# Kernel tuning notes

Hardware: AMD Instinct MI355X
Metric: run time of the kernel (lower is better)

## Reference

```python
import jax, jax.numpy as jnp
import numpy as np

M, K, N = 8192, 4096, 4096


def setup_inputs() -> dict:
    key = jax.random.key(0)
    k1, k2, k3, k4 = jax.random.split(key, 4)
    x = jax.random.normal(k1, (M, K), dtype=jnp.float32)
    # int8 weight buffer (qweight), per-output-channel dequant scales, bf16-style bias
    weight_q = jax.random.randint(k2, (N, K), -128, 128, dtype=jnp.int32).astype(jnp.int8)
    qscales = jax.random.uniform(k3, (N,), dtype=jnp.float32) * 0.01 + 0.005
    bias = jax.random.normal(k4, (N,), dtype=jnp.float32) * 0.01
    return {"x": x, "weight_q": weight_q, "qscales": qscales, "bias": bias}


def reference(x, weight_q, qscales, bias):
    # dynamic per-tensor activation quantization: clampv = max(x)
    clampv = jnp.max(x)
    x8 = jnp.clip(jnp.round(x * (127.0 / clampv)), -128, 127).astype(jnp.int8)
    acc = jax.lax.dot_general(
        x8, weight_q,
        dimension_numbers=(((1,), (1,)), ((), ())),
        preferred_element_type=jnp.int32,
    )
    # fused dequant: (acc*alpha + bias/qscales)*qscales == acc*alpha*qscales + bias
    out = acc.astype(jnp.float32) * (clampv / 127.0) * qscales[None, :] + bias[None, :]
    return out
```

## Files before the change

kernel.cpp:

```cpp
#include <hip/hip_runtime.h>
#include <math.h>

#define MDIM 8192
#define KDIM 4096
#define NDIM 4096

typedef int v4i __attribute__((ext_vector_type(4)));

__device__ __forceinline__ void gload_lds16(const void* g, void* l) {
  __builtin_amdgcn_global_load_lds(
      (const __attribute__((address_space(1))) void*)g,
      (__attribute__((address_space(3))) void*)l,
      16, 0, 0);
}

__global__ void __launch_bounds__(256) kmax(const float* __restrict__ x,
                                            unsigned int* __restrict__ key_out) {
  const int n4 = MDIM * KDIM / 4;
  int tid = blockIdx.x * blockDim.x + threadIdx.x;
  int stride = gridDim.x * blockDim.x;
  float m = -3.4e38f;
  const float4* x4 = (const float4*)x;
  for (int i = tid; i < n4; i += stride) {
    float4 v = x4[i];
    m = fmaxf(m, fmaxf(fmaxf(v.x, v.y), fmaxf(v.z, v.w)));
  }
  #pragma unroll
  for (int off = 32; off > 0; off >>= 1)
    m = fmaxf(m, __shfl_down(m, off, 64));
  __shared__ float sm[4];
  int lane = threadIdx.x & 63, wv = threadIdx.x >> 6;
  if (lane == 0) sm[wv] = m;
  __syncthreads();
  if (threadIdx.x == 0) {
    m = fmaxf(fmaxf(sm[0], sm[1]), fmaxf(sm[2], sm[3]));
    unsigned b = __float_as_uint(m);
    unsigned key = (b & 0x80000000u) ? ~b : (b | 0x80000000u);
    atomicMax(key_out, key);
  }
}

__device__ __forceinline__ float key_to_float(unsigned key) {
  unsigned b = (key & 0x80000000u) ? (key & 0x7FFFFFFFu) : ~key;
  return __uint_as_float(b);
}

__global__ void __launch_bounds__(256) kpackw(const int* __restrict__ w,
                                              signed char* __restrict__ w8) {
  __shared__ int smode;
  int ok = 1;
  #pragma unroll
  for (int i = 0; i < 16; ++i) {
    int v = w[threadIdx.x * 16 + i];
    ok &= (v >= -128) & (v <= 127);
  }
  if (threadIdx.x == 0) smode = 1;
  __syncthreads();
  if (!ok) atomicAnd(&smode, 0);
  __syncthreads();
  const int mode = smode;

  const int n16 = NDIM * KDIM / 16;
  int tid = blockIdx.x * blockDim.x + threadIdx.x;
  int stride = gridDim.x * blockDim.x;
  int4* dst = (int4*)w8;
  if (mode) {
    const int4* src = (const int4*)w;
    for (int i = tid; i < n16; i += stride) {
      int4 r;
      #pragma unroll
      for (int q = 0; q < 4; ++q) {
        int4 a = src[(size_t)i * 4 + q];
        int packed = (a.x & 255) | ((a.y & 255) << 8) |
                     ((a.z & 255) << 16) | ((a.w & 255) << 24);
        ((int*)&r)[q] = packed;
      }
      dst[i] = r;
    }
  } else {
    const int4* src = (const int4*)w;
    for (int i = tid; i < n16; i += stride) dst[i] = src[i];
  }
}

__device__ __forceinline__ int pack4(float4 v, float s) {
  int q0 = (int)fminf(fmaxf(rintf(v.x * s), -128.f), 127.f);
  int q1 = (int)fminf(fmaxf(rintf(v.y * s), -128.f), 127.f);
  int q2 = (int)fminf(fmaxf(rintf(v.z * s), -128.f), 127.f);
  int q3 = (int)fminf(fmaxf(rintf(v.w * s), -128.f), 127.f);
  return (q0 & 255) | ((q1 & 255) << 8) | ((q2 & 255) << 16) | ((q3 & 255) << 24);
}

__global__ void __launch_bounds__(256) kquant(const float* __restrict__ x,
                                              signed char* __restrict__ x8,
                                              const unsigned* __restrict__ keyp) {
  float s = 127.0f / key_to_float(*keyp);
  const int n16 = MDIM * KDIM / 16;
  int tid = blockIdx.x * blockDim.x + threadIdx.x;
  int stride = gridDim.x * blockDim.x;
  const float4* x4 = (const float4*)x;
  int4* out16 = (int4*)x8;
  for (int i = tid; i < n16; i += stride) {
    const float4* src = x4 + (size_t)i * 4;
    int4 r;
    r.x = pack4(src[0], s);
    r.y = pack4(src[1], s);
    r.z = pack4(src[2], s);
    r.w = pack4(src[3], s);
    out16[i] = r;
  }
}

constexpr int BM = 256, BN = 256, BK = 128;
constexpr int NT = KDIM / BK;

__device__ __forceinline__ v4i mfma_i8(v4i a, v4i b, v4i c) {
  return __builtin_amdgcn_mfma_i32_16x16x64_i8(a, b, c, 0, 0, 0);
}

#define PHASE_END()                                         \
  do {                                                      \
    asm volatile("s_waitcnt vmcnt(10)" ::: "memory");       \
    __builtin_amdgcn_s_barrier();                           \
    __builtin_amdgcn_sched_barrier(0);                      \
  } while (0)

__global__ void __launch_bounds__(512, 2) kgemm(
    const signed char* __restrict__ A8,
    const signed char* __restrict__ W8,
    const float* __restrict__ qs,
    const float* __restrict__ bias,
    const unsigned* __restrict__ keyp,
    float* __restrict__ out) {
  __shared__ alignas(1024) signed char lds[2][2][2][128 * 128];

  const int nbn = NDIM / BN;
  const int nwg = (MDIM / BM) * nbn;
  int bid = blockIdx.x;
  int wg = (bid & 7) * (nwg / 8) + (bid >> 3);
  const int brow = (wg / nbn) * BM;
  const int bcol = (wg % nbn) * BN;

  const int tid = threadIdx.x;
  const int lane = tid & 63;
  const int wv = tid >> 6;
  const int wr = wv >> 2, wc = wv & 3;
  const int lhi = lane >> 4, llo = lane & 15;

  const signed char* Abase = A8 + (size_t)brow * KDIM;
  const signed char* Bbase = W8 + (size_t)bcol * KDIM;

  auto stageA = [&](int t, int h) {
    signed char* dst = &lds[t & 1][0][h][0];
    const size_t k0 = (size_t)(t & (NT - 1)) * BK;
    #pragma unroll
    for (int l = 0; l < 2; ++l) {
      int p = l * 512 + tid;
      int r = p >> 3, s = p & 7;
      int R = ((r >> 6) << 7) + h * 64 + (r & 63);
      int g = s ^ (r & 7);
      gload_lds16(Abase + (size_t)R * KDIM + k0 + g * 16, dst + p * 16);
    }
  };
  auto stageB = [&](int t, int h) {
    signed char* dst = &lds[t & 1][1][h][0];
    const size_t k0 = (size_t)(t & (NT - 1)) * BK;
    #pragma unroll
    for (int l = 0; l < 2; ++l) {
      int p = l * 512 + tid;
      int r = p >> 3, s = p & 7;
      int R = ((r >> 5) << 6) + h * 32 + (r & 31);
      int g = s ^ (r & 7);
      gload_lds16(Bbase + (size_t)R * KDIM + k0 + g * 16, dst + p * 16);
    }
  };
  auto readA = [&](int par, int mi, int ks) -> v4i {
    int h = mi >> 2;
    int r = wr * 64 + (mi & 3) * 16 + llo;
    int s = (ks * 4 + lhi) ^ (llo & 7);
    return *(const v4i*)&lds[par][0][h][r * 128 + s * 16];
  };
  auto readB = [&](int par, int ni, int ks) -> v4i {
    int h = ni >> 1;
    int r = wc * 32 + (ni & 1) * 16 + llo;
    int s = (ks * 4 + lhi) ^ (llo & 7);
    return *(const v4i*)&lds[par][1][h][r * 128 + s * 16];
  };

  v4i acc[8][4];
  v4i zero = {0, 0, 0, 0};
  #pragma unroll
  for (int i = 0; i < 8; ++i)
    #pragma unroll
    for (int j = 0; j < 4; ++j) acc[i][j] = zero;

  stageA(0, 0); stageB(0, 0); stageB(0, 1); stageA(0, 1);
  stageA(1, 0); stageB(1, 0); stageB(1, 1);
  asm volatile("s_waitcnt vmcnt(6)" ::: "memory");
  __builtin_amdgcn_s_barrier();
  __builtin_amdgcn_sched_barrier(0);

  #pragma unroll 2
  for (int t = 0; t < NT; ++t) {
    const int par = t & 1;
    v4i afr03[4][2], afr47[4][2], bfr01[2][2], bfr23[2][2];

    #pragma unroll
    for (int mi = 0; mi < 4; ++mi) {
      afr03[mi][0] = readA(par, mi, 0);
      afr03[mi][1] = readA(par, mi, 1);
    }
    #pragma unroll
    for (int ni = 0; ni < 2; ++ni) {
      bfr01[ni][0] = readB(par, ni, 0);
      bfr01[ni][1] = readB(par, ni, 1);
    }
    stageA(t + 1, 1);
    __builtin_amdgcn_s_barrier();
    __builtin_amdgcn_sched_barrier(0);
    __builtin_amdgcn_s_setprio(1);
    #pragma unroll
    for (int mi = 0; mi < 4; ++mi)
      #pragma unroll
      for (int ni = 0; ni < 2; ++ni) {
        acc[mi][ni] = mfma_i8(afr03[mi][0], bfr01[ni][0], acc[mi][ni]);
        acc[mi][ni] = mfma_i8(afr03[mi][1], bfr01[ni][1], acc[mi][ni]);
      }
    __builtin_amdgcn_s_setprio(0);
    PHASE_END();

    #pragma unroll
    for (int ni = 0; ni < 2; ++ni) {
      bfr23[ni][0] = readB(par, 2 + ni, 0);
      bfr23[ni][1] = readB(par, 2 + ni, 1);
    }
    stageA(t + 2, 0);
    __builtin_amdgcn_s_barrier();
    __builtin_amdgcn_sched_barrier(0);
    __builtin_amdgcn_s_setprio(1);
    #pragma unroll
    for (int mi = 0; mi < 4; ++mi)
      #pragma unroll
      for (int ni = 0; ni < 2; ++ni) {
        acc[mi][2 + ni] = mfma_i8(afr03[mi][0], bfr23[ni][0], acc[mi][2 + ni]);
        acc[mi][2 + ni] = mfma_i8(afr03[mi][1], bfr23[ni][1], acc[mi][2 + ni]);
      }
    __builtin_amdgcn_s_setprio(0);
    PHASE_END();

    #pragma unroll
    for (int mi = 0; mi < 4; ++mi) {
      afr47[mi][0] = readA(par, 4 + mi, 0);
      afr47[mi][1] = readA(par, 4 + mi, 1);
    }
    stageB(t + 2, 0);
    __builtin_amdgcn_s_barrier();
    __builtin_amdgcn_sched_barrier(0);
    __builtin_amdgcn_s_setprio(1);
    #pragma unroll
    for (int mi = 0; mi < 4; ++mi)
      #pragma unroll
      for (int ni = 0; ni < 2; ++ni) {
        acc[4 + mi][ni] = mfma_i8(afr47[mi][0], bfr01[ni][0], acc[4 + mi][ni]);
        acc[4 + mi][ni] = mfma_i8(afr47[mi][1], bfr01[ni][1], acc[4 + mi][ni]);
      }
    __builtin_amdgcn_s_setprio(0);
    PHASE_END();

    stageB(t + 2, 1);
    __builtin_amdgcn_s_barrier();
    __builtin_amdgcn_sched_barrier(0);
    __builtin_amdgcn_s_setprio(1);
    #pragma unroll
    for (int mi = 0; mi < 4; ++mi)
      #pragma unroll
      for (int ni = 0; ni < 2; ++ni) {
        acc[4 + mi][2 + ni] = mfma_i8(afr47[mi][0], bfr23[ni][0], acc[4 + mi][2 + ni]);
        acc[4 + mi][2 + ni] = mfma_i8(afr47[mi][1], bfr23[ni][1], acc[4 + mi][2 + ni]);
      }
    __builtin_amdgcn_s_setprio(0);
    PHASE_END();
  }

  asm volatile("s_waitcnt vmcnt(0)" ::: "memory");

  const float alpha = key_to_float(*keyp) * (1.0f / 127.0f);
  #pragma unroll
  for (int ni = 0; ni < 4; ++ni) {
    int n = bcol + wc * 64 + ni * 16 + llo;
    float sc = qs[n] * alpha;
    float bv = bias[n];
    #pragma unroll
    for (int mi = 0; mi < 8; ++mi) {
      int m0 = brow + wr * 128 + mi * 16 + lhi * 4;
      #pragma unroll
      for (int j = 0; j < 4; ++j)
        out[(size_t)(m0 + j) * NDIM + n] = (float)acc[mi][ni][j] * sc + bv;
    }
  }
}

extern "C" void kernel_launch(void* const* d_in, const int* in_sizes, int n_in,
                              void* d_out, int out_size, void* d_ws, size_t ws_size,
                              hipStream_t stream) {
  const float* x = (const float*)d_in[0];
  const int* wq = (const int*)d_in[1];
  const float* qscales = (const float*)d_in[2];
  const float* bias = (const float*)d_in[3];
  float* out = (float*)d_out;

  unsigned* keyp = (unsigned*)d_ws;
  signed char* x8 = (signed char*)d_ws + 256;
  signed char* w8 = x8 + (size_t)MDIM * KDIM;

  hipMemsetAsync(keyp, 0, 4, stream);
  kpackw<<<2048, 256, 0, stream>>>(wq, w8);
  kmax<<<2048, 256, 0, stream>>>(x, keyp);
  kquant<<<2048, 256, 0, stream>>>(x, x8, keyp);
  kgemm<<<(MDIM / BM) * (NDIM / BN), 512, 0, stream>>>(x8, w8, qscales, bias, keyp, out);
}
```

Before: 223.7 us.

## Replace four-phase interleaved pipeline with simple per-iteration double-buffered prefetch

Restructures the GEMM main loop: instead of staggering half-tile global-to-LDS loads two iterations ahead across four barrier-separated MFMA phases, it now issues the whole next tile's loads at the top of each iteration, runs all MFMAs, then waits for vmcnt(0) and barriers once. This removes three barriers per iteration and the wraparound dummy loads at the end of K. In exchange, the prefetch distance drops to one tile and there is a full drain of outstanding loads every iteration, which may expose more memory latency.

```diff
diff --git a/kernel.cpp b/kernel.cpp
--- a/kernel.cpp
+++ b/kernel.cpp
@@ -114,16 +114,9 @@
 constexpr int BM = 256, BN = 256, BK = 128;
 constexpr int NT = KDIM / BK;
 
-__device__ __forceinline__ v4i mfma_i8(v4i a, v4i b, v4i c) {
+__device__ __forceinline__ v4i mfma_i8_16(v4i a, v4i b, v4i c) {
   return __builtin_amdgcn_mfma_i32_16x16x64_i8(a, b, c, 0, 0, 0);
 }
-
-#define PHASE_END()                                         \
-  do {                                                      \
-    asm volatile("s_waitcnt vmcnt(10)" ::: "memory");       \
-    __builtin_amdgcn_s_barrier();                           \
-    __builtin_amdgcn_sched_barrier(0);                      \
-  } while (0)
 
 __global__ void __launch_bounds__(512, 2) kgemm(
     const signed char* __restrict__ A8,
@@ -152,7 +145,7 @@
 
   auto stageA = [&](int t, int h) {
     signed char* dst = &lds[t & 1][0][h][0];
-    const size_t k0 = (size_t)(t & (NT - 1)) * BK;
+    const size_t k0 = (size_t)t * BK;
     #pragma unroll
     for (int l = 0; l < 2; ++l) {
       int p = l * 512 + tid;
@@ -164,7 +157,7 @@
   };
   auto stageB = [&](int t, int h) {
     signed char* dst = &lds[t & 1][1][h][0];
-    const size_t k0 = (size_t)(t & (NT - 1)) * BK;
+    const size_t k0 = (size_t)t * BK;
     #pragma unroll
     for (int l = 0; l < 2; ++l) {
       int p = l * 512 + tid;
@@ -194,9 +187,8 @@
     #pragma unroll
     for (int j = 0; j < 4; ++j) acc[i][j] = zero;
 
-  stageA(0, 0); stageB(0, 0); stageB(0, 1); stageA(0, 1);
-  stageA(1, 0); stageB(1, 0); stageB(1, 1);
-  asm volatile("s_waitcnt vmcnt(6)" ::: "memory");
+  stageA(0, 0); stageA(0, 1); stageB(0, 0); stageB(0, 1);
+  asm volatile("s_waitcnt vmcnt(0)" ::: "memory");
   __builtin_amdgcn_s_barrier();
   __builtin_amdgcn_sched_barrier(0);
 
@@ -205,6 +197,12 @@
     const int par = t & 1;
     v4i afr03[4][2], afr47[4][2], bfr01[2][2], bfr23[2][2];
 
+    if (t + 1 < NT) {
+      stageA(t + 1, 0); stageA(t + 1, 1);
+      stageB(t + 1, 0); stageB(t + 1, 1);
+    }
+    __builtin_amdgcn_sched_barrier(0);
+
     #pragma unroll
     for (int mi = 0; mi < 4; ++mi) {
       afr03[mi][0] = readA(par, mi, 0);
@@ -215,74 +213,57 @@
       bfr01[ni][0] = readB(par, ni, 0);
       bfr01[ni][1] = readB(par, ni, 1);
     }
-    stageA(t + 1, 1);
-    __builtin_amdgcn_s_barrier();
-    __builtin_amdgcn_sched_barrier(0);
     __builtin_amdgcn_s_setprio(1);
     #pragma unroll
     for (int mi = 0; mi < 4; ++mi)
       #pragma unroll
       for (int ni = 0; ni < 2; ++ni) {
-        acc[mi][ni] = mfma_i8(afr03[mi][0], bfr01[ni][0], acc[mi][ni]);
-        acc[mi][ni] = mfma_i8(afr03[mi][1], bfr01[ni][1], acc[mi][ni]);
+        acc[mi][ni] = mfma_i8_16(afr03[mi][0], bfr01[ni][0], acc[mi][ni]);
+        acc[mi][ni] = mfma_i8_16(afr03[mi][1], bfr01[ni][1], acc[mi][ni]);
       }
     __builtin_amdgcn_s_setprio(0);
-    PHASE_END();
 
     #pragma unroll
     for (int ni = 0; ni < 2; ++ni) {
       bfr23[ni][0] = readB(par, 2 + ni, 0);
       bfr23[ni][1] = readB(par, 2 + ni, 1);
     }
-    stageA(t + 2, 0);
-    __builtin_amdgcn_s_barrier();
-    __builtin_amdgcn_sched_barrier(0);
     __builtin_amdgcn_s_setprio(1);
     #pragma unroll
     for (int mi = 0; mi < 4; ++mi)
       #pragma unroll
       for (int ni = 0; ni < 2; ++ni) {
-        acc[mi][2 + ni] = mfma_i8(afr03[mi][0], bfr23[ni][0], acc[mi][2 + ni]);
-        acc[mi][2 + ni] = mfma_i8(afr03[mi][1], bfr23[ni][1], acc[mi][2 + ni]);
+        acc[mi][2 + ni] = mfma_i8_16(afr03[mi][0], bfr23[ni][0], acc[mi][2 + ni]);
+        acc[mi][2 + ni] = mfma_i8_16(afr03[mi][1], bfr23[ni][1], acc[mi][2 + ni]);
       }
     __builtin_amdgcn_s_setprio(0);
-    PHASE_END();
 
     #pragma unroll
     for (int mi = 0; mi < 4; ++mi) {
       afr47[mi][0] = readA(par, 4 + mi, 0);
       afr47[mi][1] = readA(par, 4 + mi, 1);
     }
-    stageB(t + 2, 0);
+    __builtin_amdgcn_s_setprio(1);
+    #pragma unroll
+    for (int mi = 0; mi < 4; ++mi)
+      #pragma unroll
+      for (int ni = 0; ni < 2; ++ni) {
+        acc[4 + mi][ni] = mfma_i8_16(afr47[mi][0], bfr01[ni][0], acc[4 + mi][ni]);
+        acc[4 + mi][ni] = mfma_i8_16(afr47[mi][1], bfr01[ni][1], acc[4 + mi][ni]);
+      }
+    #pragma unroll
+    for (int mi = 0; mi < 4; ++mi)
+      #pragma unroll
+      for (int ni = 0; ni < 2; ++ni) {
+        acc[4 + mi][2 + ni] = mfma_i8_16(afr47[mi][0], bfr23[ni][0], acc[4 + mi][2 + ni]);
+        acc[4 + mi][2 + ni] = mfma_i8_16(afr47[mi][1], bfr23[ni][1], acc[4 + mi][2 + ni]);
+      }
+    __builtin_amdgcn_s_setprio(0);
+
+    asm volatile("s_waitcnt vmcnt(0)" ::: "memory");
     __builtin_amdgcn_s_barrier();
     __builtin_amdgcn_sched_barrier(0);
-    __builtin_amdgcn_s_setprio(1);
-    #pragma unroll
-    for (int mi = 0; mi < 4; ++mi)
-      #pragma unroll
-      for (int ni = 0; ni < 2; ++ni) {
-        acc[4 + mi][ni] = mfma_i8(afr47[mi][0], bfr01[ni][0], acc[4 + mi][ni]);
-        acc[4 + mi][ni] = mfma_i8(afr47[mi][1], bfr01[ni][1], acc[4 + mi][ni]);
-      }
-    __builtin_amdgcn_s_setprio(0);
-    PHASE_END();
-
-    stageB(t + 2, 1);
-    __builtin_amdgcn_s_barrier();
-    __builtin_amdgcn_sched_barrier(0);
-    __builtin_amdgcn_s_setprio(1);
-    #pragma unroll
-    for (int mi = 0; mi < 4; ++mi)
-      #pragma unroll
-      for (int ni = 0; ni < 2; ++ni) {
-        acc[4 + mi][2 + ni] = mfma_i8(afr47[mi][0], bfr23[ni][0], acc[4 + mi][2 + ni]);
-        acc[4 + mi][2 + ni] = mfma_i8(afr47[mi][1], bfr23[ni][1], acc[4 + mi][2 + ni]);
-      }
-    __builtin_amdgcn_s_setprio(0);
-    PHASE_END();
-  }
-
-  asm volatile("s_waitcnt vmcnt(0)" ::: "memory");
+  }
 
   const float alpha = key_to_float(*keyp) * (1.0f / 127.0f);
   #pragma unroll
@@ -313,7 +294,7 @@
   signed char* x8 = (signed char*)d_ws + 256;
   signed char* w8 = x8 + (size_t)MDIM * KDIM;
 
-  hipMemsetAsync(keyp, 0, 4, stream);
+  (void)hipMemsetAsync(keyp, 0, 4, stream);
   kpackw<<<2048, 256, 0, stream>>>(wq, w8);
   kmax<<<2048, 256, 0, stream>>>(x, keyp);
   kquant<<<2048, 256, 0, stream>>>(x, x8, keyp);
```

New measurement: 222.7 us. No clear change (-0.5%).
